# Optimization experiments

Measured on AMD Instinct MI355X. Metric: run time of the kernel, lower is better.

The kernel has to match this reference:

```python
import jax, jax.numpy as jnp
import numpy as np
from math import sqrt

B, LQ, LKV = 4, 1024, 1024
QD = KD = VD = 1024
MODEL_DIM = 1024
H = 16
HD = MODEL_DIM // H  # per-head model_dim = 64


def setup_inputs() -> dict:
    key = jax.random.key(0)
    ks = jax.random.split(key, 10)
    s = 0.02
    return {
        "queries": jax.random.normal(ks[0], (B, LQ, QD), jnp.float32),
        "context": jax.random.normal(ks[1], (B, LKV, KD), jnp.float32),
        # stacked per-head linear weights (torch Linear: y = x @ W.T + b); store as [H, in, out]
        "Wq": jax.random.normal(ks[2], (H, QD, HD), jnp.float32) * s,
        "bq": jax.random.normal(ks[3], (H, HD), jnp.float32) * s,
        "Wk": jax.random.normal(ks[4], (KD, HD * 1 * H), jnp.float32).reshape(H, KD, HD) * s,
        "bk": jax.random.normal(ks[5], (H, HD), jnp.float32) * s,
        "Wv": jax.random.normal(ks[6], (H, VD, HD), jnp.float32) * s,
        "bv": jax.random.normal(ks[7], (H, HD), jnp.float32) * s,
        "Wo": jax.random.normal(ks[8], (H * HD, MODEL_DIM), jnp.float32) * s,
        "bo": jax.random.normal(ks[9], (MODEL_DIM,), jnp.float32) * s,
    }


def reference(queries, context, Wq, bq, Wk, bk, Wv, bv, Wo, bo):
    # queries: [B,Lq,Dq]; context: [B,Lkv,Dk]
    # Per-head projections, batched over heads (equivalent to the torch per-head loop).
    q = jnp.einsum("bld,hdm->bhlm", queries, Wq) + bq[None, :, None, :]  # [B,H,Lq,hd]
    k = jnp.einsum("bld,hdm->bhlm", context, Wk) + bk[None, :, None, :]  # [B,H,Lkv,hd]
    v = jnp.einsum("bld,hdm->bhlm", context, Wv) + bv[None, :, None, :]  # [B,H,Lkv,hd]

    scale = 1.0 / sqrt(HD)
    scores = jnp.einsum("bhqd,bhkd->bhqk", q, k) * scale  # [B,H,Lq,Lkv]
    att = jax.nn.softmax(scores, axis=-1)
    head_out = jnp.einsum("bhqk,bhkd->bhqd", att, v)  # [B,H,Lq,hd]

    # torch concatenates heads along the last dim in head order 0..H-1
    multi = head_out.transpose(0, 2, 1, 3).reshape(B, LQ, H * HD)
    residual = q.transpose(0, 2, 1, 3).reshape(B, LQ, H * HD)

    out = multi @ Wo + bo  # [B,Lq,model_dim]
    return out, residual
```

## Files before the change

kernel.cpp:

```cpp
#include <hip/hip_runtime.h>
#include <hip/hip_bf16.h>


typedef unsigned short u16;
typedef __attribute__((ext_vector_type(8))) short short8;
typedef __attribute__((ext_vector_type(4))) float f32x4;

__device__ __forceinline__ float bf2f(u16 u) {
    union { unsigned int i; float f; } c;
    c.i = ((unsigned int)u) << 16;
    return c.f;
}

__device__ __forceinline__ u16 f2bf(float f) {
    unsigned int x = __float_as_uint(f);
    unsigned int r = (x + 0x7fffu + ((x >> 16) & 1u)) >> 16;
    return (u16)r;
}

__device__ __forceinline__ void glds16(u16* lds, const u16* g) {
    __builtin_amdgcn_global_load_lds(
        (const __attribute__((address_space(1))) void*)g,
        (__attribute__((address_space(3))) void*)lds, 16, 0, 0);
}

#define FENCE() asm volatile("" ::: "memory")
#define BAR() do { FENCE(); __builtin_amdgcn_s_barrier(); FENCE(); } while (0)
#define WAIT_LGKM0() do { asm volatile("s_waitcnt lgkmcnt(0)" ::: "memory"); \
                          __builtin_amdgcn_sched_barrier(0); } while (0)
#define WAIT_VM6() do { asm volatile("s_waitcnt vmcnt(6)" ::: "memory"); \
                        __builtin_amdgcn_sched_barrier(0); } while (0)
#define WAIT_VM4() do { asm volatile("s_waitcnt vmcnt(4)" ::: "memory"); \
                        __builtin_amdgcn_sched_barrier(0); } while (0)
#define WAIT_VM0() do { asm volatile("s_waitcnt vmcnt(0)" ::: "memory"); \
                        __builtin_amdgcn_sched_barrier(0); } while (0)

__global__ __launch_bounds__(256) void prep(
    const float* __restrict__ q, const float* __restrict__ ctx,
    const float* __restrict__ Wq, const float* __restrict__ Wk,
    const float* __restrict__ Wv, const float* __restrict__ Wo,
    u16* __restrict__ Aq, u16* __restrict__ Ac,
    u16* __restrict__ Wqt, u16* __restrict__ Wkt,
    u16* __restrict__ Wvt, u16* __restrict__ Wot)
{
    __shared__ float ls[64][65];
    const int t = threadIdx.x;
    int bid = blockIdx.x;

    if (bid < 4096) {
        const float* in = (bid < 2048) ? q : ctx;
        u16* out = (bid < 2048) ? Aq : Ac;
        size_t i = ((size_t)(bid & 2047) * 256 + t) * 8;
        float4 v0 = *(const float4*)(in + i);
        float4 v1 = *(const float4*)(in + i + 4);
        short8 p;
        p[0] = (short)f2bf(v0.x); p[1] = (short)f2bf(v0.y);
        p[2] = (short)f2bf(v0.z); p[3] = (short)f2bf(v0.w);
        p[4] = (short)f2bf(v1.x); p[5] = (short)f2bf(v1.y);
        p[6] = (short)f2bf(v1.z); p[7] = (short)f2bf(v1.w);
        *(short8*)(out + i) = p;
        return;
    }
    bid -= 4096;
    const float* in; u16* out; int C; size_t moff; int rt, ct;
    if (bid < 768) {
        const int m = bid >> 8, idx = bid & 255;
        in = (m == 0) ? Wq : (m == 1) ? Wk : Wv;
        out = (m == 0) ? Wqt : (m == 1) ? Wkt : Wvt;
        C = 64; rt = (idx & 15) * 64; ct = 0; moff = (size_t)(idx >> 4) * 65536;
    } else {
        const int idx = bid - 768;
        in = Wo; out = Wot; C = 1024; moff = 0;
        rt = (idx & 15) * 64; ct = (idx >> 4) * 64;
    }
    #pragma unroll
    for (int i = 0; i < 4; ++i) {
        int s = i * 256 + t;
        int row = s >> 4, chunk = s & 15;
        float4 v = *(const float4*)(in + moff + (size_t)(rt + row) * C + ct + chunk * 4);
        ls[row][chunk * 4 + 0] = v.x;
        ls[row][chunk * 4 + 1] = v.y;
        ls[row][chunk * 4 + 2] = v.z;
        ls[row][chunk * 4 + 3] = v.w;
    }
    __syncthreads();
    #pragma unroll
    for (int i = 0; i < 2; ++i) {
        int s = i * 256 + t;
        int n = s >> 3, kc = s & 7;
        short8 p;
        #pragma unroll
        for (int j = 0; j < 8; ++j) p[j] = (short)f2bf(ls[kc * 8 + j][n]);
        *(short8*)(out + moff + (size_t)(ct + n) * 1024 + rt + kc * 8) = p;
    }
}

__global__ __launch_bounds__(512) void gemm_qkv8(
    const u16* __restrict__ Aq, const u16* __restrict__ Ac,
    const u16* __restrict__ Wqt, const u16* __restrict__ Wkt,
    const u16* __restrict__ Wvt,
    const float* __restrict__ bq, const float* __restrict__ bk,
    const float* __restrict__ bv,
    u16* __restrict__ qws, u16* __restrict__ kws, u16* __restrict__ vtws)
{
    __shared__ u16 lds[2][2][256 * 64];

    const int tid = threadIdx.x;
    const int w = tid >> 6, lane = tid & 63;
    const int wr = w >> 2, wc = w & 3;
    const int quad = lane >> 4, c = lane & 15, cx = c & 7;
    const int sr = tid >> 3;
    const int gch = (tid & 7) ^ (sr & 7);

    const int f = blockIdx.x;
    const int xcd = f & 7, r = f >> 3;
    const int z = r >> 3;
    const int mt = xcd * 2 + ((r >> 2) & 1);
    const int nt = r & 3;
    const int m0 = mt * 256, n0 = nt * 256;

    const u16* A = (z == 0) ? Aq : Ac;
    const u16* Wt = (z == 0) ? Wqt : (z == 1) ? Wkt : Wvt;
    const float* bias = (z == 0) ? bq : (z == 1) ? bk : bv;

    const u16* gAt = A + (size_t)(m0 + sr) * 1024 + gch * 8;
    const u16* gBt = Wt + (size_t)(n0 + sr) * 1024 + gch * 8;

    auto stageA = [&](int par, int half, int t) {
        const u16* g = gAt + (size_t)half * 128 * 1024 + t * 64;
        u16* l = &lds[par][0][(half * 128 + w * 8) * 64];
        glds16(l, g);
        glds16(l + 64 * 64, g + (size_t)64 * 1024);
    };
    auto stageB = [&](int par, int half, int t) {
        const u16* g = gBt + (size_t)half * 128 * 1024 + t * 64;
        u16* l = &lds[par][1][(half * 128 + w * 8) * 64];
        glds16(l, g);
        glds16(l + 64 * 64, g + (size_t)64 * 1024);
    };

    f32x4 acc[8][4] = {};
    short8 aq[4][2], bA[2][2], bB[2][2];

    auto ldA = [&](int par, int mh) {
        #pragma unroll
        for (int mf = 0; mf < 4; ++mf)
            #pragma unroll
            for (int ks = 0; ks < 2; ++ks)
                aq[mf][ks] = *(const short8*)&lds[par][0][
                    (wr * 128 + mh * 64 + mf * 16 + c) * 64 + (((ks * 4 + quad) ^ cx) * 8)];
    };
    auto ldB = [&](int par, int nh, short8 (&bq_)[2][2]) {
        #pragma unroll
        for (int nf = 0; nf < 2; ++nf)
            #pragma unroll
            for (int ks = 0; ks < 2; ++ks)
                bq_[nf][ks] = *(const short8*)&lds[par][1][
                    (wc * 64 + nh * 32 + nf * 16 + c) * 64 + (((ks * 4 + quad) ^ cx) * 8)];
    };
    auto mma = [&](int mh, int nh, short8 (&bq_)[2][2]) {
        #pragma unroll
        for (int mf = 0; mf < 4; ++mf)
            #pragma unroll
            for (int nf = 0; nf < 2; ++nf)
                #pragma unroll
                for (int ks = 0; ks < 2; ++ks)
                    acc[mh * 4 + mf][nh * 2 + nf] =
                        __builtin_amdgcn_mfma_f32_16x16x32_bf16(
                            aq[mf][ks], bq_[nf][ks], acc[mh * 4 + mf][nh * 2 + nf], 0, 0, 0);
    };

    stageB(0, 0, 0); stageB(0, 1, 0); stageA(0, 0, 0); stageA(0, 1, 0);
    stageB(1, 0, 1); stageB(1, 1, 1);
    WAIT_VM4(); BAR();

    #pragma unroll 1
    for (int i = 0; i < 8; ++i) {
        const int o = 2 * i + 1, e = 2 * i + 2;

        ldA(0, 0); ldB(0, 0, bA);
        stageA(1, 0, o);
        BAR(); WAIT_LGKM0();
        __builtin_amdgcn_s_setprio(1); mma(0, 0, bA); __builtin_amdgcn_s_setprio(0);
        BAR();
        ldB(0, 1, bB);
        stageA(1, 1, o);
        BAR(); WAIT_LGKM0();
        __builtin_amdgcn_s_setprio(1); mma(0, 1, bB); __builtin_amdgcn_s_setprio(0);
        BAR();
        ldA(0, 1);
        if (i < 7) stageB(0, 0, e);
        BAR(); WAIT_LGKM0();
        __builtin_amdgcn_s_setprio(1); mma(1, 1, bB); __builtin_amdgcn_s_setprio(0);
        BAR();
        if (i < 7) stageB(0, 1, e);
        BAR();
        __builtin_amdgcn_s_setprio(1); mma(1, 0, bA); __builtin_amdgcn_s_setprio(0);
        if (i < 7) { WAIT_VM4(); } else { WAIT_VM0(); }
        BAR();
        ldA(1, 0); ldB(1, 0, bA);
        if (i < 7) stageA(0, 0, e);
        BAR(); WAIT_LGKM0();
        __builtin_amdgcn_s_setprio(1); mma(0, 0, bA); __builtin_amdgcn_s_setprio(0);
        BAR();
        ldB(1, 1, bB);
        if (i < 7) stageA(0, 1, e);
        BAR(); WAIT_LGKM0();
        __builtin_amdgcn_s_setprio(1); mma(0, 1, bB); __builtin_amdgcn_s_setprio(0);
        BAR();
        ldA(1, 1);
        if (i < 7) stageB(1, 0, e + 1);
        BAR(); WAIT_LGKM0();
        __builtin_amdgcn_s_setprio(1); mma(1, 1, bB); __builtin_amdgcn_s_setprio(0);
        BAR();
        if (i < 7) stageB(1, 1, e + 1);
        BAR();
        __builtin_amdgcn_s_setprio(1); mma(1, 0, bA); __builtin_amdgcn_s_setprio(0);
        if (i < 7) WAIT_VM4();
        BAR();
    }

    const int h = nt * 4 + wc;
    const int b = m0 >> 10;
    const int lbase = (m0 & 1023) + wr * 128;

    float bb[4];
    #pragma unroll
    for (int cn = 0; cn < 4; ++cn)
        bb[cn] = bias[h * 64 + (cn >> 1) * 32 + (cn & 1) * 16 + c];

    if (z < 2) {
        u16* dst = (z == 0) ? qws : kws;
        const float scale = (z == 0) ? 0.125f : 1.0f;
        u16* dbase = dst + (size_t)(b * 16 + h) * 1024 * 64;
        #pragma unroll
        for (int mi = 0; mi < 8; ++mi) {
            const int ro = (mi >> 2) * 64 + (mi & 3) * 16;
            const int rowb = lbase + ro + quad * 4;
            #pragma unroll
            for (int rr = 0; rr < 4; ++rr) {
                u16* drow = dbase + (size_t)(rowb + rr) * 64;
                #pragma unroll
                for (int cn = 0; cn < 4; ++cn) {
                    const int hd = (cn >> 1) * 32 + (cn & 1) * 16 + c;
                    drow[hd] = f2bf((acc[mi][cn][rr] + bb[cn]) * scale);
                }
            }
        }
    } else {
        u16* dbase = vtws + (size_t)(b * 16 + h) * 64 * 1024;
        #pragma unroll
        for (int mi = 0; mi < 8; ++mi) {
            const int ro = (mi >> 2) * 64 + (mi & 3) * 16;
            const int l0 = lbase + ro + quad * 4;
            #pragma unroll
            for (int cn = 0; cn < 4; ++cn) {
                const int hd = (cn >> 1) * 32 + (cn & 1) * 16 + c;
                ushort4 pk;
                pk.x = f2bf(acc[mi][cn][0] + bb[cn]);
                pk.y = f2bf(acc[mi][cn][1] + bb[cn]);
                pk.z = f2bf(acc[mi][cn][2] + bb[cn]);
                pk.w = f2bf(acc[mi][cn][3] + bb[cn]);
                *(ushort4*)(dbase + (size_t)hd * 1024 + l0) = pk;
            }
        }
    }
}

__global__ __launch_bounds__(256) void gemm_out(
    const u16* __restrict__ A, const u16* __restrict__ Wot,
    const float* __restrict__ bo, float* __restrict__ out)
{
    __shared__ u16 As[2][128 * 64];
    __shared__ u16 Bs[2][64 * 64];
    const int f = blockIdx.x;
    const int xcd = f & 7, k = f >> 3;
    const int m0 = (xcd * 4 + (k & 3)) * 128;
    const int n0 = (k >> 2) * 64;
    const int t = threadIdx.x;
    const int w = t >> 6, lane = t & 63;
    const int quad = lane >> 4, c = lane & 15;
    const int cx = c & 7;

    const int sr = w * 8 + (lane >> 3);
    const int gch = (lane & 7) ^ ((lane >> 3) & 7);
    const u16* gA = A + (size_t)(m0 + sr) * 1024 + gch * 8;
    const u16* gB = Wot + (size_t)(n0 + sr) * 1024 + gch * 8;

    const int arow = (w >> 1) * 64 + c;
    const int brow = (w & 1) * 32 + c;

    auto stage = [&](int par, int kt) {
        #pragma unroll
        for (int i = 0; i < 4; ++i)
            glds16(As[par] + (i * 32 + w * 8) * 64, gA + (size_t)i * 32 * 1024 + kt);
        #pragma unroll
        for (int i = 0; i < 2; ++i)
            glds16(Bs[par] + (i * 32 + w * 8) * 64, gB + (size_t)i * 32 * 1024 + kt);
    };

    f32x4 acc[4][2] = {};
    stage(0, 0);
    stage(1, 64);
    #pragma unroll 1
    for (int i = 0; i < 16; ++i) {
        const int cur = i & 1;
        if (i < 15) { WAIT_VM6(); } else { WAIT_VM0(); }
        BAR();
        #pragma unroll
        for (int kh = 0; kh < 2; ++kh) {
            const int ch = (kh * 4 + quad);
            short8 af[4], bf[2];
            #pragma unroll
            for (int rs = 0; rs < 4; ++rs)
                af[rs] = *(const short8*)(As[cur] + (arow + rs * 16) * 64 + (ch ^ cx) * 8);
            #pragma unroll
            for (int cs = 0; cs < 2; ++cs)
                bf[cs] = *(const short8*)(Bs[cur] + (brow + cs * 16) * 64 + (ch ^ cx) * 8);
            #pragma unroll
            for (int rs = 0; rs < 4; ++rs)
                #pragma unroll
                for (int cs = 0; cs < 2; ++cs)
                    acc[rs][cs] = __builtin_amdgcn_mfma_f32_16x16x32_bf16(
                        af[rs], bf[cs], acc[rs][cs], 0, 0, 0);
        }
        BAR();
        if (i < 14) stage(cur, (i + 2) * 64);
    }

    const int nb = n0 + (w & 1) * 32;
    float bb[2];
    #pragma unroll
    for (int cs = 0; cs < 2; ++cs) bb[cs] = bo[nb + cs * 16 + c];

    #pragma unroll
    for (int rs = 0; rs < 4; ++rs) {
        #pragma unroll
        for (int r = 0; r < 4; ++r) {
            const int row = m0 + (w >> 1) * 64 + rs * 16 + quad * 4 + r;
            float* orow = out + (size_t)row * 1024 + nb;
            #pragma unroll
            for (int cs = 0; cs < 2; ++cs)
                orow[cs * 16 + c] = acc[rs][cs][r] + bb[cs];
        }
    }
}

__global__ __launch_bounds__(256) void attn_mfma(
    const u16* __restrict__ qws, const u16* __restrict__ kws,
    const u16* __restrict__ vtws, u16* __restrict__ multi,
    float* __restrict__ resid)
{
    __shared__ u16 Ks[2][64 * 64];
    __shared__ u16 Vs[2][64 * 64];
    __shared__ u16 Ps[4][16 * 64];
    const int t = threadIdx.x;
    const int wave = t >> 6, lane = t & 63;
    const int quad = lane >> 4, c = lane & 15;
    const int cx = c & 7;
    const int f = blockIdx.x;
    const int xcd = f & 7, j = f >> 3;
    const int bh = xcd * 8 + (j & 7);
    const int qt = j >> 3;
    const int b = bh >> 4, h = bh & 15;
    const int q0 = qt * 64 + wave * 16;

    const u16* qb = qws + ((size_t)bh * 1024 + q0) * 64;
    const u16* kb = kws + (size_t)bh * 65536;
    const u16* vb = vtws + (size_t)bh * 65536;

    short8 qa0 = *(const short8*)(qb + (size_t)c * 64 + quad * 8);
    short8 qa1 = *(const short8*)(qb + (size_t)c * 64 + 32 + quad * 8);

    const int srow = wave * 16 + (lane >> 3);
    const int gch = (lane & 7) ^ ((lane >> 3) & 7);
    const u16* gK0 = kb + (size_t)srow * 64 + gch * 8;
    const u16* gK1 = kb + (size_t)(srow + 8) * 64 + gch * 8;
    const u16* gV0 = vb + (size_t)srow * 1024 + gch * 8;
    const u16* gV1 = vb + (size_t)(srow + 8) * 1024 + gch * 8;

    auto stage = [&](int par, int kt) {
        glds16(Ks[par] + (wave * 16) * 64,     gK0 + (size_t)kt * 64);
        glds16(Ks[par] + (wave * 16 + 8) * 64, gK1 + (size_t)kt * 64);
        glds16(Vs[par] + (wave * 16) * 64,     gV0 + kt);
        glds16(Vs[par] + (wave * 16 + 8) * 64, gV1 + kt);
    };

    f32x4 O[4] = {};
    float ps[4] = {0.f, 0.f, 0.f, 0.f};
    u16* pw = &Ps[wave][0];

    stage(0, 0);
    stage(1, 64);

    #pragma unroll 1
    for (int i = 0; i < 16; ++i) {
        const int cur = i & 1;
        if (i < 15) { WAIT_VM4(); } else { WAIT_VM0(); }
        BAR();

        const u16* Kc = Ks[cur];
        const u16* Vc = Vs[cur];

        f32x4 s[4];
        __builtin_amdgcn_s_setprio(1);
        #pragma unroll
        for (int nt = 0; nt < 4; ++nt) {
            const u16* kr = Kc + (nt * 16 + c) * 64;
            short8 kb0 = *(const short8*)(kr + ((quad ^ cx)) * 8);
            short8 kb1 = *(const short8*)(kr + (((4 + quad) ^ cx)) * 8);
            f32x4 z = {};
            z = __builtin_amdgcn_mfma_f32_16x16x32_bf16(qa0, kb0, z, 0, 0, 0);
            z = __builtin_amdgcn_mfma_f32_16x16x32_bf16(qa1, kb1, z, 0, 0, 0);
            s[nt] = z;
        }
        __builtin_amdgcn_s_setprio(0);

        #pragma unroll
        for (int nt = 0; nt < 4; ++nt)
            #pragma unroll
            for (int r = 0; r < 4; ++r) {
                float p = __expf(s[nt][r]);
                ps[r] += p;
                const int prow = quad * 4 + r;
                pw[prow * 64 + (((nt * 2 + (c >> 3)) ^ (prow & 7)) * 8) + (c & 7)]
                    = (u16)(__float_as_uint(p) >> 16);
            }
        short8 pa0 = *(const short8*)(pw + c * 64 + ((quad ^ cx)) * 8);
        short8 pa1 = *(const short8*)(pw + c * 64 + (((4 + quad) ^ cx)) * 8);

        __builtin_amdgcn_s_setprio(1);
        #pragma unroll
        for (int nt = 0; nt < 4; ++nt) {
            const u16* vr = Vc + (nt * 16 + c) * 64;
            short8 vb0 = *(const short8*)(vr + ((quad ^ cx)) * 8);
            short8 vb1 = *(const short8*)(vr + (((4 + quad) ^ cx)) * 8);
            O[nt] = __builtin_amdgcn_mfma_f32_16x16x32_bf16(pa0, vb0, O[nt], 0, 0, 0);
            O[nt] = __builtin_amdgcn_mfma_f32_16x16x32_bf16(pa1, vb1, O[nt], 0, 0, 0);
        }
        __builtin_amdgcn_s_setprio(0);

        BAR();
        if (i < 14) stage(cur, (i + 2) * 64);
    }

    float inv[4];
    #pragma unroll
    for (int r = 0; r < 4; ++r) {
        float sum = ps[r];
        sum += __shfl_xor(sum, 1);
        sum += __shfl_xor(sum, 2);
        sum += __shfl_xor(sum, 4);
        sum += __shfl_xor(sum, 8);
        inv[r] = 1.0f / sum;
    }

    u16* ob = multi + ((size_t)b * 1024 + q0 + quad * 4) * 1024 + h * 64 + c;
    #pragma unroll
    for (int r = 0; r < 4; ++r) {
        u16* orow = ob + (size_t)r * 1024;
        orow[0]  = f2bf(O[0][r] * inv[r]);
        orow[16] = f2bf(O[1][r] * inv[r]);
        orow[32] = f2bf(O[2][r] * inv[r]);
        orow[48] = f2bf(O[3][r] * inv[r]);
    }

    float* rr = resid + ((size_t)b * 1024 + q0 + c) * 1024 + h * 64;
    #pragma unroll
    for (int jj = 0; jj < 8; ++jj) {
        rr[quad * 8 + jj]      = bf2f((u16)qa0[jj]) * 8.0f;
        rr[32 + quad * 8 + jj] = bf2f((u16)qa1[jj]) * 8.0f;
    }
}

extern "C" void kernel_launch(void* const* d_in, const int* in_sizes, int n_in,
                              void* d_out, int out_size, void* d_ws, size_t ws_size,
                              hipStream_t stream) {
    const float* queries = (const float*)d_in[0];
    const float* context = (const float*)d_in[1];
    const float* Wq = (const float*)d_in[2];
    const float* bq = (const float*)d_in[3];
    const float* Wk = (const float*)d_in[4];
    const float* bk = (const float*)d_in[5];
    const float* Wv = (const float*)d_in[6];
    const float* bv = (const float*)d_in[7];
    const float* Wo = (const float*)d_in[8];
    const float* bo = (const float*)d_in[9];

    float* out = (float*)d_out;
    float* resid = out + (size_t)4 * 1024 * 1024;

    const size_t M1 = 1024 * 1024;
    u16* Aq   = (u16*)d_ws;
    u16* Ac   = Aq + 4 * M1;
    u16* Wqt  = Ac + 4 * M1;
    u16* Wkt  = Wqt + M1;
    u16* Wvt  = Wkt + M1;
    u16* Wot  = Wvt + M1;
    u16* qws  = Wot + M1;
    u16* kws  = qws + 4 * M1;
    u16* vtws = kws + 4 * M1;
    u16* mws  = vtws + 4 * M1;

    prep<<<5120, 256, 0, stream>>>(queries, context, Wq, Wk, Wv, Wo,
                                   Aq, Ac, Wqt, Wkt, Wvt, Wot);
    gemm_qkv8<<<192, 512, 0, stream>>>(Aq, Ac, Wqt, Wkt, Wvt,
                                       bq, bk, bv, qws, kws, vtws);
    attn_mfma<<<1024, 256, 0, stream>>>(qws, kws, vtws, mws, resid);
    gemm_out<<<512, 256, 0, stream>>>(mws, Wot, bo, out);
}
```

Baseline: 192.1 us.

## Process four query row blocks per wave in attention to reuse K/V tiles

Each wave now handles 64 query rows (four 16-row blocks) instead of 16, so every K/V tile staged in shared memory and loaded into registers is reused four times. The grid shrinks from 1024 to 256 blocks and launch bounds request one block per CU. This cuts global-to-LDS traffic and LDS reads of K/V per query row. The cost is higher register pressure (Q fragments, K/V fragments and four accumulator sets) and fewer blocks, which leaves less parallelism to hide latency.

```diff
diff --git a/kernel.cpp b/kernel.cpp
--- a/kernel.cpp
+++ b/kernel.cpp
@@ -346,7 +346,7 @@
     }
 }
 
-__global__ __launch_bounds__(256) void attn_mfma(
+__global__ __launch_bounds__(256, 1) void attn_mfma(
     const u16* __restrict__ qws, const u16* __restrict__ kws,
     const u16* __restrict__ vtws, u16* __restrict__ multi,
     float* __restrict__ resid)
@@ -363,14 +363,18 @@
     const int bh = xcd * 8 + (j & 7);
     const int qt = j >> 3;
     const int b = bh >> 4, h = bh & 15;
-    const int q0 = qt * 64 + wave * 16;
+    const int q0 = qt * 256 + wave * 64;
 
     const u16* qb = qws + ((size_t)bh * 1024 + q0) * 64;
     const u16* kb = kws + (size_t)bh * 65536;
     const u16* vb = vtws + (size_t)bh * 65536;
 
-    short8 qa0 = *(const short8*)(qb + (size_t)c * 64 + quad * 8);
-    short8 qa1 = *(const short8*)(qb + (size_t)c * 64 + 32 + quad * 8);
+    short8 qa[4][2];
+    #pragma unroll
+    for (int rb = 0; rb < 4; ++rb) {
+        qa[rb][0] = *(const short8*)(qb + (size_t)(rb * 16 + c) * 64 + quad * 8);
+        qa[rb][1] = *(const short8*)(qb + (size_t)(rb * 16 + c) * 64 + 32 + quad * 8);
+    }
 
     const int srow = wave * 16 + (lane >> 3);
     const int gch = (lane & 7) ^ ((lane >> 3) & 7);
@@ -386,8 +390,8 @@
         glds16(Vs[par] + (wave * 16 + 8) * 64, gV1 + kt);
     };
 
-    f32x4 O[4] = {};
-    float ps[4] = {0.f, 0.f, 0.f, 0.f};
+    f32x4 O[4][4] = {};
+    float ps[4][4] = {};
     u16* pw = &Ps[wave][0];
 
     stage(0, 0);
@@ -402,74 +406,84 @@
         const u16* Kc = Ks[cur];
         const u16* Vc = Vs[cur];
 
-        f32x4 s[4];
-        __builtin_amdgcn_s_setprio(1);
+        short8 kf[4][2], vf[4][2];
         #pragma unroll
         for (int nt = 0; nt < 4; ++nt) {
             const u16* kr = Kc + (nt * 16 + c) * 64;
-            short8 kb0 = *(const short8*)(kr + ((quad ^ cx)) * 8);
-            short8 kb1 = *(const short8*)(kr + (((4 + quad) ^ cx)) * 8);
-            f32x4 z = {};
-            z = __builtin_amdgcn_mfma_f32_16x16x32_bf16(qa0, kb0, z, 0, 0, 0);
-            z = __builtin_amdgcn_mfma_f32_16x16x32_bf16(qa1, kb1, z, 0, 0, 0);
-            s[nt] = z;
-        }
-        __builtin_amdgcn_s_setprio(0);
-
-        #pragma unroll
-        for (int nt = 0; nt < 4; ++nt)
-            #pragma unroll
-            for (int r = 0; r < 4; ++r) {
-                float p = __expf(s[nt][r]);
-                ps[r] += p;
-                const int prow = quad * 4 + r;
-                pw[prow * 64 + (((nt * 2 + (c >> 3)) ^ (prow & 7)) * 8) + (c & 7)]
-                    = (u16)(__float_as_uint(p) >> 16);
+            kf[nt][0] = *(const short8*)(kr + ((quad ^ cx)) * 8);
+            kf[nt][1] = *(const short8*)(kr + (((4 + quad) ^ cx)) * 8);
+            const u16* vr = Vc + (nt * 16 + c) * 64;
+            vf[nt][0] = *(const short8*)(vr + ((quad ^ cx)) * 8);
+            vf[nt][1] = *(const short8*)(vr + (((4 + quad) ^ cx)) * 8);
+        }
+
+        #pragma unroll
+        for (int rb = 0; rb < 4; ++rb) {
+            f32x4 s[4];
+            __builtin_amdgcn_s_setprio(1);
+            #pragma unroll
+            for (int nt = 0; nt < 4; ++nt) {
+                f32x4 z = {};
+                z = __builtin_amdgcn_mfma_f32_16x16x32_bf16(qa[rb][0], kf[nt][0], z, 0, 0, 0);
+                z = __builtin_amdgcn_mfma_f32_16x16x32_bf16(qa[rb][1], kf[nt][1], z, 0, 0, 0);
+                s[nt] = z;
             }
-        short8 pa0 = *(const short8*)(pw + c * 64 + ((quad ^ cx)) * 8);
-        short8 pa1 = *(const short8*)(pw + c * 64 + (((4 + quad) ^ cx)) * 8);
-
-        __builtin_amdgcn_s_setprio(1);
-        #pragma unroll
-        for (int nt = 0; nt < 4; ++nt) {
-            const u16* vr = Vc + (nt * 16 + c) * 64;
-            short8 vb0 = *(const short8*)(vr + ((quad ^ cx)) * 8);
-            short8 vb1 = *(const short8*)(vr + (((4 + quad) ^ cx)) * 8);
-            O[nt] = __builtin_amdgcn_mfma_f32_16x16x32_bf16(pa0, vb0, O[nt], 0, 0, 0);
-            O[nt] = __builtin_amdgcn_mfma_f32_16x16x32_bf16(pa1, vb1, O[nt], 0, 0, 0);
-        }
-        __builtin_amdgcn_s_setprio(0);
+            __builtin_amdgcn_s_setprio(0);
+
+            #pragma unroll
+            for (int nt = 0; nt < 4; ++nt)
+                #pragma unroll
+                for (int r = 0; r < 4; ++r) {
+                    float p = __expf(s[nt][r]);
+                    ps[rb][r] += p;
+                    const int prow = quad * 4 + r;
+                    pw[prow * 64 + (((nt * 2 + (c >> 3)) ^ (prow & 7)) * 8) + (c & 7)]
+                        = (u16)(__float_as_uint(p) >> 16);
+                }
+            short8 pa0 = *(const short8*)(pw + c * 64 + ((quad ^ cx)) * 8);
+            short8 pa1 = *(const short8*)(pw + c * 64 + (((4 + quad) ^ cx)) * 8);
+
+            __builtin_amdgcn_s_setprio(1);
+            #pragma unroll
+            for (int nt = 0; nt < 4; ++nt) {
+                O[rb][nt] = __builtin_amdgcn_mfma_f32_16x16x32_bf16(pa0, vf[nt][0], O[rb][nt], 0, 0, 0);
+                O[rb][nt] = __builtin_amdgcn_mfma_f32_16x16x32_bf16(pa1, vf[nt][1], O[rb][nt], 0, 0, 0);
+            }
+            __builtin_amdgcn_s_setprio(0);
+        }
 
         BAR();
         if (i < 14) stage(cur, (i + 2) * 64);
     }
 
-    float inv[4];
-    #pragma unroll
-    for (int r = 0; r < 4; ++r) {
-        float sum = ps[r];
-        sum += __shfl_xor(sum, 1);
-        sum += __shfl_xor(sum, 2);
-        sum += __shfl_xor(sum, 4);
-        sum += __shfl_xor(sum, 8);
-        inv[r] = 1.0f / sum;
-    }
-
-    u16* ob = multi + ((size_t)b * 1024 + q0 + quad * 4) * 1024 + h * 64 + c;
-    #pragma unroll
-    for (int r = 0; r < 4; ++r) {
-        u16* orow = ob + (size_t)r * 1024;
-        orow[0]  = f2bf(O[0][r] * inv[r]);
-        orow[16] = f2bf(O[1][r] * inv[r]);
-        orow[32] = f2bf(O[2][r] * inv[r]);
-        orow[48] = f2bf(O[3][r] * inv[r]);
-    }
-
-    float* rr = resid + ((size_t)b * 1024 + q0 + c) * 1024 + h * 64;
-    #pragma unroll
-    for (int jj = 0; jj < 8; ++jj) {
-        rr[quad * 8 + jj]      = bf2f((u16)qa0[jj]) * 8.0f;
-        rr[32 + quad * 8 + jj] = bf2f((u16)qa1[jj]) * 8.0f;
+    #pragma unroll
+    for (int rb = 0; rb < 4; ++rb) {
+        float inv[4];
+        #pragma unroll
+        for (int r = 0; r < 4; ++r) {
+            float sum = ps[rb][r];
+            sum += __shfl_xor(sum, 1);
+            sum += __shfl_xor(sum, 2);
+            sum += __shfl_xor(sum, 4);
+            sum += __shfl_xor(sum, 8);
+            inv[r] = 1.0f / sum;
+        }
+        u16* ob = multi + ((size_t)b * 1024 + q0 + rb * 16 + quad * 4) * 1024 + h * 64 + c;
+        #pragma unroll
+        for (int r = 0; r < 4; ++r) {
+            u16* orow = ob + (size_t)r * 1024;
+            orow[0]  = f2bf(O[rb][0][r] * inv[r]);
+            orow[16] = f2bf(O[rb][1][r] * inv[r]);
+            orow[32] = f2bf(O[rb][2][r] * inv[r]);
+            orow[48] = f2bf(O[rb][3][r] * inv[r]);
+        }
+
+        float* rr = resid + ((size_t)b * 1024 + q0 + rb * 16 + c) * 1024 + h * 64;
+        #pragma unroll
+        for (int jj = 0; jj < 8; ++jj) {
+            rr[quad * 8 + jj]      = bf2f((u16)qa[rb][0][jj]) * 8.0f;
+            rr[32 + quad * 8 + jj] = bf2f((u16)qa[rb][1][jj]) * 8.0f;
+        }
     }
 }
 
@@ -506,6 +520,6 @@
                                    Aq, Ac, Wqt, Wkt, Wvt, Wot);
     gemm_qkv8<<<192, 512, 0, stream>>>(Aq, Ac, Wqt, Wkt, Wvt,
                                        bq, bk, bv, qws, kws, vtws);
-    attn_mfma<<<1024, 256, 0, stream>>>(qws, kws, vtws, mws, resid);
+    attn_mfma<<<256, 256, 0, stream>>>(qws, kws, vtws, mws, resid);
     gemm_out<<<512, 256, 0, stream>>>(mws, Wot, bo, out);
 }
```

Result: slower. 199.5 us (+3.9%).
